# Kernel tuning notes

Hardware: AMD Instinct MI355X
Metric: run time of the kernel (lower is better)

Reference implementation:

```python
import jax, jax.numpy as jnp
import numpy as np

B, T, C = 2, 2048, 1024
N = 16
D = C // N  # 64


def setup_inputs() -> dict:
    key = jax.random.key(0)
    ks = jax.random.split(key, 5)
    s = 1.0 / np.sqrt(C)  # lecun_normal-ish scale for Dense kernels
    return {
        "src": jax.random.normal(ks[0], (B, T, C), jnp.float32),
        "mask": jnp.ones((B, T), jnp.float32),  # unused on causal path
        "Wq": jax.random.normal(ks[1], (C, C), jnp.float32) * s,
        "bq": jnp.zeros((C,), jnp.float32),
        "Wk": jax.random.normal(ks[2], (C, C), jnp.float32) * s,
        "bk": jnp.zeros((C,), jnp.float32),
        "Wv": jax.random.normal(ks[3], (C, C), jnp.float32) * s,
        "bv": jnp.zeros((C,), jnp.float32),
        "Wo": jax.random.normal(ks[4], (C, C), jnp.float32) * s,
        "bo": jnp.zeros((C,), jnp.float32),
    }


def reference(src, mask, Wq, bq, Wk, bk, Wv, bv, Wo, bo):
    # QKV projections -> [B, N, T, D]
    def heads(x):
        return x.reshape(B, T, N, D).transpose(0, 2, 1, 3)

    q = heads(src @ Wq + bq)
    k = heads(src @ Wk + bk)
    v = heads(src @ Wv + bv)

    # scores [B, N, T, T], causal mask, softmax
    scores = jnp.einsum("bntd,bnsd->bnts", q, k) / jnp.sqrt(jnp.float32(D))
    causal = jnp.tril(jnp.ones((T, T), bool))
    scores = jnp.where(causal, scores, -jnp.inf)
    attn = jax.nn.softmax(scores, axis=-1)

    # weighted values, merge heads, output projection (dropout deterministic)
    out = jnp.einsum("bnts,bnsd->bntd", attn, v)
    out = out.transpose(0, 2, 1, 3).reshape(B, T, C)
    return out @ Wo + bo
```

## Files before the change

kernel.cpp:

```cpp
#include <hip/hip_runtime.h>

typedef __bf16 bf16;
typedef bf16 bf16x8 __attribute__((ext_vector_type(8)));
typedef float f32x4 __attribute__((ext_vector_type(4)));
typedef unsigned short u16;
typedef u16 u16x4 __attribute__((ext_vector_type(4)));
typedef u16 u16x8 __attribute__((ext_vector_type(8)));

typedef const __attribute__((address_space(1))) void* gptr_t;
typedef __attribute__((address_space(3))) void* sptr_t;

__device__ __forceinline__ void async16(const void* g, void* l) {
  __builtin_amdgcn_global_load_lds((gptr_t)g, (sptr_t)l, 16, 0, 0);
}
__device__ __forceinline__ u16 f2bf(float v) {
  return __builtin_bit_cast(u16, (bf16)v);
}

__device__ __forceinline__ size_t paddr(int r, int k, int KT) {
  return (size_t)((r >> 4) * KT + (k >> 5)) * 512 + ((k >> 3) & 3) * 128 +
         (r & 15) * 8 + (k & 7);
}

__global__ void kPrep(const float* __restrict__ src, u16* __restrict__ Xp,
                      const float* __restrict__ Wq, const float* __restrict__ Wk,
                      const float* __restrict__ Wv, const float* __restrict__ Wo,
                      u16* __restrict__ Wp) {
  __shared__ float tile[32][33];
  const int bid = blockIdx.x, tid = threadIdx.x;
  if (bid < 4096) {
    const int i = (bid * 256 + tid) * 4;
    const int m = i >> 10, k = i & 1023;
    float4 v = *(const float4*)&src[i];
    u16x4 o = {f2bf(v.x), f2bf(v.y), f2bf(v.z), f2bf(v.w)};
    *(u16x4*)&Xp[paddr(m, k, 32)] = o;
  } else {
    const int t = bid - 4096;
    const int z = t >> 10, tt = t & 1023;
    const float* W = (z == 0) ? Wq : (z == 1) ? Wk : (z == 2) ? Wv : Wo;
    const int n0 = (tt & 31) * 32, k0 = (tt >> 5) * 32;
    const int tx = tid & 31, ty = tid >> 5;
#pragma unroll
    for (int j = 0; j < 4; ++j)
      tile[ty + j * 8][tx] = W[(size_t)(k0 + ty + j * 8) * 1024 + n0 + tx];
    __syncthreads();
    if (tid < 128) {
      const int sub = tid >> 6, l = tid & 63, hi = l >> 4, lo = l & 15;
      u16x8 o;
#pragma unroll
      for (int e = 0; e < 8; ++e) o[e] = f2bf(tile[hi * 8 + e][sub * 16 + lo]);
      const size_t ad = (size_t)z * 1048576 +
                        (size_t)(((n0 >> 4) + sub) * 32 + (k0 >> 5)) * 512 +
                        hi * 128 + lo * 8;
      *(u16x8*)&Wp[ad] = o;
    }
  }
}

__global__ __launch_bounds__(256, 3) void kGemmQKV(
    const u16* __restrict__ A, const u16* __restrict__ Bt,
    const float* __restrict__ b0, const float* __restrict__ b1,
    const float* __restrict__ b2, u16* __restrict__ outQ) {
  __shared__ __align__(16) u16 Als[2][8 * 512];
  const int tid = threadIdx.x, l = tid & 63, w = tid >> 6;
  const int bid = (blockIdx.x & 7) * 96 + (blockIdx.x >> 3);
  const int mb = bid & 31, nb = bid >> 5;
  const int mbase = mb * 128, nbase = nb * 128;
  const int wr = (w >> 1) * 64, wc = (w & 1) * 64;
  const int hi = l >> 4, lo = l & 15;

  const u16* bb[4];
#pragma unroll
  for (int nf = 0; nf < 4; ++nf)
    bb[nf] = &Bt[(size_t)((nbase + wc + nf * 16) >> 4) * 16384 + l * 8];

  f32x4 acc[4][4];
#pragma unroll
  for (int i = 0; i < 4; ++i)
#pragma unroll
    for (int j = 0; j < 4; ++j) acc[i][j] = (f32x4){0.f, 0.f, 0.f, 0.f};

  auto stageA = [&](int bufi, int kt) {
#pragma unroll
    for (int i = 0; i < 2; ++i) {
      const int fr = w * 2 + i;
      async16(&A[(size_t)((mb * 8 + fr) * 32 + kt) * 512 + l * 8],
              &Als[bufi][fr * 512]);
    }
  };

  bf16x8 breg[2][4];
  stageA(0, 0);
#pragma unroll
  for (int nf = 0; nf < 4; ++nf) breg[0][nf] = *(const bf16x8*)&bb[nf][0];

  auto step = [&](int kt, bf16x8 (&bc)[4], bf16x8 (&bn)[4]) {
    const int cur = kt & 1;
    if (kt < 31) {
      stageA(cur ^ 1, kt + 1);
#pragma unroll
      for (int nf = 0; nf < 4; ++nf)
        bn[nf] = *(const bf16x8*)&bb[nf][(kt + 1) * 512];
      asm volatile("s_waitcnt vmcnt(6)" ::: "memory");
    } else {
      asm volatile("s_waitcnt vmcnt(0)" ::: "memory");
    }
    __builtin_amdgcn_s_barrier();
    __builtin_amdgcn_sched_barrier(0);

    bf16x8 a[4];
#pragma unroll
    for (int mf = 0; mf < 4; ++mf)
      a[mf] = *(const bf16x8*)&Als[cur][((w >> 1) * 4 + mf) * 512 + l * 8];
#pragma unroll
    for (int mf = 0; mf < 4; ++mf)
#pragma unroll
      for (int nf = 0; nf < 4; ++nf)
        acc[mf][nf] = __builtin_amdgcn_mfma_f32_16x16x32_bf16(a[mf], bc[nf],
                                                              acc[mf][nf], 0, 0, 0);
    __builtin_amdgcn_s_barrier();
  };

  for (int kt2 = 0; kt2 < 32; kt2 += 2) {
    step(kt2, breg[0], breg[1]);
    step(kt2 + 1, breg[1], breg[0]);
  }

  u16* Qo = outQ;
  u16* Ko = outQ + 4 * 1048576;
  u16* Vo = outQ + 8 * 1048576;
  const int mat = nb >> 3;
  const float* bias = (mat == 0) ? b0 : (mat == 1) ? b1 : b2;
  const float qs = (mat == 0) ? 0.1803368801f : 1.0f;
#pragma unroll
  for (int nf = 0; nf < 4; ++nf) {
    const int n = nbase + wc + nf * 16 + lo;
    const int cc = n & 1023, h = cc >> 6, d = cc & 63;
    const float bsv = bias[cc];
#pragma unroll
    for (int mf = 0; mf < 4; ++mf)
#pragma unroll
      for (int r = 0; r < 4; ++r) {
        const int m = mbase + wr + mf * 16 + hi * 4 + r;
        const int bb_ = m >> 11, t = m & 2047;
        const u16 hv = f2bf((acc[mf][nf][r] + bsv) * qs);
        const size_t hd = (size_t)(bb_ * 16 + h) * 131072;
        if (mat < 2) {
          (mat == 0 ? Qo : Ko)[hd + paddr(t, d, 2)] = hv;
        } else {
          Vo[hd + paddr(d, t, 64)] = hv;
        }
      }
  }
}

__global__ __launch_bounds__(256, 2) void kGemmO(
    const u16* __restrict__ A, const u16* __restrict__ Bt,
    const float* __restrict__ b0, float* __restrict__ outF) {
  __shared__ __align__(16) u16 Als[2][8 * 512];
  const int tid = threadIdx.x, l = tid & 63, w = tid >> 6;
  const int bid = (blockIdx.x & 7) * 64 + (blockIdx.x >> 3);
  const int mb = bid & 31, nb = bid >> 5;
  const int mbase = mb * 128, nbase = nb * 64;
  const int wr = (w >> 1) * 64, wc = (w & 1) * 32;
  const int hi = l >> 4, lo = l & 15;

  const u16* bb[2];
#pragma unroll
  for (int nf = 0; nf < 2; ++nf)
    bb[nf] = &Bt[(size_t)((nbase + wc + nf * 16) >> 4) * 16384 + l * 8];

  f32x4 acc[4][2];
#pragma unroll
  for (int i = 0; i < 4; ++i)
#pragma unroll
    for (int j = 0; j < 2; ++j) acc[i][j] = (f32x4){0.f, 0.f, 0.f, 0.f};

  auto stageA = [&](int bufi, int kt) {
#pragma unroll
    for (int i = 0; i < 2; ++i) {
      const int fr = w * 2 + i;
      async16(&A[(size_t)((mb * 8 + fr) * 32 + kt) * 512 + l * 8],
              &Als[bufi][fr * 512]);
    }
  };

  bf16x8 breg[2][2];
  stageA(0, 0);
#pragma unroll
  for (int nf = 0; nf < 2; ++nf) breg[0][nf] = *(const bf16x8*)&bb[nf][0];

  auto step = [&](int kt, bf16x8 (&bc)[2], bf16x8 (&bn)[2]) {
    const int cur = kt & 1;
    if (kt < 31) {
      stageA(cur ^ 1, kt + 1);
#pragma unroll
      for (int nf = 0; nf < 2; ++nf)
        bn[nf] = *(const bf16x8*)&bb[nf][(kt + 1) * 512];
      asm volatile("s_waitcnt vmcnt(4)" ::: "memory");
    } else {
      asm volatile("s_waitcnt vmcnt(0)" ::: "memory");
    }
    __builtin_amdgcn_s_barrier();
    __builtin_amdgcn_sched_barrier(0);

    bf16x8 a[4];
#pragma unroll
    for (int mf = 0; mf < 4; ++mf)
      a[mf] = *(const bf16x8*)&Als[cur][((w >> 1) * 4 + mf) * 512 + l * 8];
#pragma unroll
    for (int mf = 0; mf < 4; ++mf)
#pragma unroll
      for (int nf = 0; nf < 2; ++nf)
        acc[mf][nf] = __builtin_amdgcn_mfma_f32_16x16x32_bf16(a[mf], bc[nf],
                                                              acc[mf][nf], 0, 0, 0);
    __builtin_amdgcn_s_barrier();
  };

  for (int kt2 = 0; kt2 < 32; kt2 += 2) {
    step(kt2, breg[0], breg[1]);
    step(kt2 + 1, breg[1], breg[0]);
  }

#pragma unroll
  for (int nf = 0; nf < 2; ++nf) {
    const int n = nbase + wc + nf * 16 + lo;
    const float bsv = b0[n];
#pragma unroll
    for (int mf = 0; mf < 4; ++mf)
#pragma unroll
      for (int r = 0; r < 4; ++r) {
        const int m = mbase + wr + mf * 16 + hi * 4 + r;
        outF[(size_t)m * 1024 + n] = acc[mf][nf][r] + bsv;
      }
  }
}

#define PSTR 36
__global__ __launch_bounds__(512, 4) void kAttn(const u16* __restrict__ Qp,
                                                const u16* __restrict__ Kp,
                                                const u16* __restrict__ Vp,
                                                u16* __restrict__ AOp) {
  __shared__ __align__(16) u16 Pl[8][16 * PSTR];
  __shared__ __align__(16) float Red[4][2][16][64];
  __shared__ float RedL[4][2][64];
  const int tid = threadIdx.x, l = tid & 63, w = tid >> 6;
  const int grp = w >> 1, half = w & 1;
  const int g = l >> 4, c = l & 15;
  const int pi = blockIdx.x, bh = blockIdx.y;
  const int qtA = pi, qtB = 31 - pi;
  const size_t head = (size_t)bh * 131072;
  const u16* Kh = Kp + head;
  const u16* Vh = Vp + head;

  bf16x8 aqA[2], aqB[2];
#pragma unroll
  for (int ks = 0; ks < 2; ++ks) {
    aqA[ks] = *(const bf16x8*)&Qp[head + (size_t)((qtA * 4 + grp) * 2 + ks) * 512 + l * 8];
    aqB[ks] = *(const bf16x8*)&Qp[head + (size_t)((qtB * 4 + grp) * 2 + ks) * 512 + l * 8];
  }

  f32x4 accA[4], accB[4];
#pragma unroll
  for (int i = 0; i < 4; ++i) {
    accA[i] = (f32x4){0.f, 0.f, 0.f, 0.f};
    accB[i] = (f32x4){0.f, 0.f, 0.f, 0.f};
  }
  float lA_ = 0.f, lB_ = 0.f;

  bf16x8 kr[4];
#pragma unroll
  for (int f = 0; f < 4; ++f)
    kr[f] = *(const bf16x8*)&Kh[(size_t)((half * 2 + (f >> 1)) * 2 + (f & 1)) * 512 + l * 8];
  bf16x8 vr[4];

  auto finishTile = [&](const f32x4* sT, bool diag, f32x4* accO, float& lpart) {
    float v[8];
#pragma unroll
    for (int sf = 0; sf < 2; ++sf)
#pragma unroll
      for (int r = 0; r < 4; ++r) v[sf * 4 + r] = sT[sf][r];
    if (diag) {
      const int qin = grp * 16 + c;
#pragma unroll
      for (int sf = 0; sf < 2; ++sf)
#pragma unroll
        for (int r = 0; r < 4; ++r)
          if (half * 32 + sf * 16 + g * 4 + r > qin) v[sf * 4 + r] = -__builtin_inff();
    }
    float p[8];
#pragma unroll
    for (int i = 0; i < 8; ++i) p[i] = __builtin_exp2f(v[i]);
#pragma unroll
    for (int sf = 0; sf < 2; ++sf) {
      u16x4 q4 = {f2bf(p[sf * 4 + 0]), f2bf(p[sf * 4 + 1]),
                  f2bf(p[sf * 4 + 2]), f2bf(p[sf * 4 + 3])};
      *(u16x4*)&Pl[w][c * PSTR + sf * 16 + g * 4] = q4;
    }
    lpart += ((p[0] + p[1]) + (p[2] + p[3])) + ((p[4] + p[5]) + (p[6] + p[7]));
    bf16x8 pf = *(const bf16x8*)&Pl[w][c * PSTR + g * 8];
#pragma unroll
    for (int nd = 0; nd < 4; ++nd)
      accO[nd] = __builtin_amdgcn_mfma_f32_16x16x32_bf16(pf, vr[nd], accO[nd], 0, 0, 0);
  };

  for (int st = 0; st <= qtB; ++st) {
#pragma unroll
    for (int nd = 0; nd < 4; ++nd)
      vr[nd] = *(const bf16x8*)&Vh[(size_t)(nd * 64 + st * 2 + half) * 512 + l * 8];
    const bool pair = (st <= qtA);

    f32x4 sB[2], sA[2];
#pragma unroll
    for (int i = 0; i < 2; ++i) {
      sB[i] = (f32x4){0.f, 0.f, 0.f, 0.f};
      sA[i] = (f32x4){0.f, 0.f, 0.f, 0.f};
    }
#pragma unroll
    for (int sf = 0; sf < 2; ++sf)
#pragma unroll
      for (int ks = 0; ks < 2; ++ks)
        sB[sf] = __builtin_amdgcn_mfma_f32_16x16x32_bf16(kr[sf * 2 + ks], aqB[ks],
                                                         sB[sf], 0, 0, 0);
    if (pair)
#pragma unroll
      for (int sf = 0; sf < 2; ++sf)
#pragma unroll
        for (int ks = 0; ks < 2; ++ks)
          sA[sf] = __builtin_amdgcn_mfma_f32_16x16x32_bf16(kr[sf * 2 + ks], aqA[ks],
                                                           sA[sf], 0, 0, 0);
    if (st < qtB) {
#pragma unroll
      for (int f = 0; f < 4; ++f)
        kr[f] = *(const bf16x8*)&Kh[(size_t)(((st + 1) * 4 + half * 2 + (f >> 1)) * 2 +
                                             (f & 1)) * 512 + l * 8];
    }
    finishTile(sB, st == qtB, accB, lB_);
    if (pair) finishTile(sA, st == qtA, accA, lA_);
  }

  float lcB = lB_ + __shfl_xor(lB_, 16);
  lcB += __shfl_xor(lcB, 32);
  float lcA = lA_ + __shfl_xor(lA_, 16);
  lcA += __shfl_xor(lcA, 32);
  __syncthreads();
  if (half) {
#pragma unroll
    for (int nd = 0; nd < 4; ++nd)
#pragma unroll
      for (int r = 0; r < 4; ++r) {
        Red[grp][0][nd * 4 + r][l] = accB[nd][r];
        Red[grp][1][nd * 4 + r][l] = accA[nd][r];
      }
    RedL[grp][0][l] = lcB;
    RedL[grp][1][l] = lcA;
  }
  __syncthreads();
  if (!half) {
#pragma unroll
    for (int nd = 0; nd < 4; ++nd)
#pragma unroll
      for (int r = 0; r < 4; ++r) {
        accB[nd][r] += Red[grp][0][nd * 4 + r][l];
        accA[nd][r] += Red[grp][1][nd * 4 + r][l];
      }
    lcB += RedL[grp][0][l];
    lcA += RedL[grp][1][l];

    const int b = bh >> 4, h = bh & 15;
    auto writeOut = [&](int qt, f32x4* accO, float lc) {
#pragma unroll
      for (int r = 0; r < 4; ++r) {
        const float lr = __shfl(lc, g * 4 + r);
        const float rin = 1.0f / lr;
        const int mg = b * 2048 + qt * 64 + grp * 16 + g * 4 + r;
#pragma unroll
        for (int nd = 0; nd < 4; ++nd) {
          const int col = h * 64 + nd * 16 + c;
          AOp[paddr(mg, col, 32)] = f2bf(accO[nd][r] * rin);
        }
      }
    };
    writeOut(qtB, accB, lcB);
    writeOut(qtA, accA, lcA);
  }
}

extern "C" void kernel_launch(void* const* d_in, const int* in_sizes, int n_in,
                              void* d_out, int out_size, void* d_ws, size_t ws_size,
                              hipStream_t stream) {
  const float* src = (const float*)d_in[0];
  const float* Wq = (const float*)d_in[2];
  const float* bq = (const float*)d_in[3];
  const float* Wk = (const float*)d_in[4];
  const float* bk = (const float*)d_in[5];
  const float* Wv = (const float*)d_in[6];
  const float* bv = (const float*)d_in[7];
  const float* Wo = (const float*)d_in[8];
  const float* bo = (const float*)d_in[9];
  float* out = (float*)d_out;

  char* ws = (char*)d_ws;
  u16* Wp = (u16*)(ws);
  u16* Xp = (u16*)(ws + 8ull * 1024 * 1024);
  u16* Qb = (u16*)(ws + 16ull * 1024 * 1024);
  u16* AOp = (u16*)(ws + 40ull * 1024 * 1024);

  kPrep<<<dim3(8192), dim3(256), 0, stream>>>(src, Xp, Wq, Wk, Wv, Wo, Wp);
  kGemmQKV<<<dim3(768), dim3(256), 0, stream>>>(Xp, Wp, bq, bk, bv, Qb);
  kAttn<<<dim3(16, 32), dim3(512), 0, stream>>>(Qb, Qb + 4 * 1048576,
                                                Qb + 8 * 1048576, AOp);
  kGemmO<<<dim3(512), dim3(256), 0, stream>>>(AOp, Wp + 3ull * 1048576, bo, out);
}
```

Baseline: 116.7 us.

## Process four query tiles per attention block to reuse K/V loads

Each attention block now handles four causally balanced query tiles (pi, 15-pi, 16+pi, 31-pi) instead of two, so every K and V fragment loaded from global memory feeds up to four QK and PV tile computations. The grid shrinks from 512 to 256 blocks and uses a 1D index that maps heads across XCDs so blocks sharing a head stay on the same XCD's L2. Launch bounds drop to 2 blocks per CU to make room for the extra Q fragments and accumulators. The cost is fewer resident waves and a smaller grid, which may reduce latency hiding and leave CUs idle.

```diff
diff --git a/kernel.cpp b/kernel.cpp
--- a/kernel.cpp
+++ b/kernel.cpp
@@ -237,7 +237,7 @@
 }
 
 #define PSTR 36
-__global__ __launch_bounds__(512, 4) void kAttn(const u16* __restrict__ Qp,
+__global__ __launch_bounds__(512, 2) void kAttn(const u16* __restrict__ Qp,
                                                 const u16* __restrict__ Kp,
                                                 const u16* __restrict__ Vp,
                                                 u16* __restrict__ AOp) {
@@ -247,32 +247,47 @@
   const int tid = threadIdx.x, l = tid & 63, w = tid >> 6;
   const int grp = w >> 1, half = w & 1;
   const int g = l >> 4, c = l & 15;
-  const int pi = blockIdx.x, bh = blockIdx.y;
-  const int qtA = pi, qtB = 31 - pi;
+  const int id = blockIdx.x;
+  const int xcd = id & 7, rem = id >> 3;
+  const int pi = rem & 7, bh = (rem >> 3) * 8 + xcd;
+  const int qt0 = 31 - pi, qt1 = 16 + pi, qt2 = 15 - pi, qt3 = pi;
   const size_t head = (size_t)bh * 131072;
   const u16* Kh = Kp + head;
   const u16* Vh = Vp + head;
 
-  bf16x8 aqA[2], aqB[2];
+  bf16x8 aq0[2], aq1[2], aq2[2], aq3[2];
 #pragma unroll
   for (int ks = 0; ks < 2; ++ks) {
-    aqA[ks] = *(const bf16x8*)&Qp[head + (size_t)((qtA * 4 + grp) * 2 + ks) * 512 + l * 8];
-    aqB[ks] = *(const bf16x8*)&Qp[head + (size_t)((qtB * 4 + grp) * 2 + ks) * 512 + l * 8];
-  }
-
-  f32x4 accA[4], accB[4];
+    aq0[ks] = *(const bf16x8*)&Qp[head + (size_t)((qt0 * 4 + grp) * 2 + ks) * 512 + l * 8];
+    aq1[ks] = *(const bf16x8*)&Qp[head + (size_t)((qt1 * 4 + grp) * 2 + ks) * 512 + l * 8];
+    aq2[ks] = *(const bf16x8*)&Qp[head + (size_t)((qt2 * 4 + grp) * 2 + ks) * 512 + l * 8];
+    aq3[ks] = *(const bf16x8*)&Qp[head + (size_t)((qt3 * 4 + grp) * 2 + ks) * 512 + l * 8];
+  }
+
+  f32x4 acc0[4], acc1[4], acc2[4], acc3[4];
 #pragma unroll
   for (int i = 0; i < 4; ++i) {
-    accA[i] = (f32x4){0.f, 0.f, 0.f, 0.f};
-    accB[i] = (f32x4){0.f, 0.f, 0.f, 0.f};
-  }
-  float lA_ = 0.f, lB_ = 0.f;
+    acc0[i] = (f32x4){0.f, 0.f, 0.f, 0.f};
+    acc1[i] = (f32x4){0.f, 0.f, 0.f, 0.f};
+    acc2[i] = (f32x4){0.f, 0.f, 0.f, 0.f};
+    acc3[i] = (f32x4){0.f, 0.f, 0.f, 0.f};
+  }
+  float l0 = 0.f, l1 = 0.f, l2 = 0.f, l3 = 0.f;
 
   bf16x8 kr[4];
 #pragma unroll
   for (int f = 0; f < 4; ++f)
     kr[f] = *(const bf16x8*)&Kh[(size_t)((half * 2 + (f >> 1)) * 2 + (f & 1)) * 512 + l * 8];
   bf16x8 vr[4];
+
+  auto qkTile = [&](const bf16x8* aq, f32x4* sT) {
+#pragma unroll
+    for (int sf = 0; sf < 2; ++sf)
+#pragma unroll
+      for (int ks = 0; ks < 2; ++ks)
+        sT[sf] = __builtin_amdgcn_mfma_f32_16x16x32_bf16(kr[sf * 2 + ks], aq[ks],
+                                                         sT[sf], 0, 0, 0);
+  };
 
   auto finishTile = [&](const f32x4* sT, bool diag, f32x4* accO, float& lpart) {
     float v[8];
@@ -304,86 +319,92 @@
       accO[nd] = __builtin_amdgcn_mfma_f32_16x16x32_bf16(pf, vr[nd], accO[nd], 0, 0, 0);
   };
 
-  for (int st = 0; st <= qtB; ++st) {
+  const int nst = qt0 + 1;
+  for (int st = 0; st < nst; ++st) {
 #pragma unroll
     for (int nd = 0; nd < 4; ++nd)
       vr[nd] = *(const bf16x8*)&Vh[(size_t)(nd * 64 + st * 2 + half) * 512 + l * 8];
-    const bool pair = (st <= qtA);
-
-    f32x4 sB[2], sA[2];
-#pragma unroll
-    for (int i = 0; i < 2; ++i) {
-      sB[i] = (f32x4){0.f, 0.f, 0.f, 0.f};
-      sA[i] = (f32x4){0.f, 0.f, 0.f, 0.f};
-    }
-#pragma unroll
-    for (int sf = 0; sf < 2; ++sf)
-#pragma unroll
-      for (int ks = 0; ks < 2; ++ks)
-        sB[sf] = __builtin_amdgcn_mfma_f32_16x16x32_bf16(kr[sf * 2 + ks], aqB[ks],
-                                                         sB[sf], 0, 0, 0);
-    if (pair)
-#pragma unroll
-      for (int sf = 0; sf < 2; ++sf)
-#pragma unroll
-        for (int ks = 0; ks < 2; ++ks)
-          sA[sf] = __builtin_amdgcn_mfma_f32_16x16x32_bf16(kr[sf * 2 + ks], aqA[ks],
-                                                           sA[sf], 0, 0, 0);
-    if (st < qtB) {
-#pragma unroll
-      for (int f = 0; f < 4; ++f)
-        kr[f] = *(const bf16x8*)&Kh[(size_t)(((st + 1) * 4 + half * 2 + (f >> 1)) * 2 +
-                                             (f & 1)) * 512 + l * 8];
-    }
-    finishTile(sB, st == qtB, accB, lB_);
-    if (pair) finishTile(sA, st == qtA, accA, lA_);
-  }
-
-  float lcB = lB_ + __shfl_xor(lB_, 16);
-  lcB += __shfl_xor(lcB, 32);
-  float lcA = lA_ + __shfl_xor(lA_, 16);
-  lcA += __shfl_xor(lcA, 32);
-  __syncthreads();
-  if (half) {
-#pragma unroll
-    for (int nd = 0; nd < 4; ++nd)
-#pragma unroll
-      for (int r = 0; r < 4; ++r) {
-        Red[grp][0][nd * 4 + r][l] = accB[nd][r];
-        Red[grp][1][nd * 4 + r][l] = accA[nd][r];
+
+    f32x4 sT[2];
+    if (st <= qt3) {
+#pragma unroll
+      for (int i = 0; i < 2; ++i) sT[i] = (f32x4){0.f, 0.f, 0.f, 0.f};
+      qkTile(aq3, sT);
+      finishTile(sT, st == qt3, acc3, l3);
+    }
+    if (st <= qt2) {
+#pragma unroll
+      for (int i = 0; i < 2; ++i) sT[i] = (f32x4){0.f, 0.f, 0.f, 0.f};
+      qkTile(aq2, sT);
+      finishTile(sT, st == qt2, acc2, l2);
+    }
+    if (st <= qt1) {
+#pragma unroll
+      for (int i = 0; i < 2; ++i) sT[i] = (f32x4){0.f, 0.f, 0.f, 0.f};
+      qkTile(aq1, sT);
+      finishTile(sT, st == qt1, acc1, l1);
+    }
+    {
+#pragma unroll
+      for (int i = 0; i < 2; ++i) sT[i] = (f32x4){0.f, 0.f, 0.f, 0.f};
+      qkTile(aq0, sT);
+      if (st < qt0) {
+#pragma unroll
+        for (int f = 0; f < 4; ++f)
+          kr[f] = *(const bf16x8*)&Kh[(size_t)(((st + 1) * 4 + half * 2 + (f >> 1)) * 2 +
+                                               (f & 1)) * 512 + l * 8];
       }
-    RedL[grp][0][l] = lcB;
-    RedL[grp][1][l] = lcA;
-  }
-  __syncthreads();
-  if (!half) {
-#pragma unroll
-    for (int nd = 0; nd < 4; ++nd)
-#pragma unroll
-      for (int r = 0; r < 4; ++r) {
-        accB[nd][r] += Red[grp][0][nd * 4 + r][l];
-        accA[nd][r] += Red[grp][1][nd * 4 + r][l];
+      finishTile(sT, st == qt0, acc0, l0);
+    }
+  }
+
+  const int b = bh >> 4, h = bh & 15;
+  auto writeOut = [&](int qt, const f32x4* accO, float lc) {
+#pragma unroll
+    for (int r = 0; r < 4; ++r) {
+      const float lr = __shfl(lc, g * 4 + r);
+      const float rin = 1.0f / lr;
+      const int mg = b * 2048 + qt * 64 + grp * 16 + g * 4 + r;
+#pragma unroll
+      for (int nd = 0; nd < 4; ++nd) {
+        const int col = h * 64 + nd * 16 + c;
+        AOp[paddr(mg, col, 32)] = f2bf(accO[nd][r] * rin);
       }
-    lcB += RedL[grp][0][l];
-    lcA += RedL[grp][1][l];
-
-    const int b = bh >> 4, h = bh & 15;
-    auto writeOut = [&](int qt, f32x4* accO, float lc) {
-#pragma unroll
-      for (int r = 0; r < 4; ++r) {
-        const float lr = __shfl(lc, g * 4 + r);
-        const float rin = 1.0f / lr;
-        const int mg = b * 2048 + qt * 64 + grp * 16 + g * 4 + r;
-#pragma unroll
-        for (int nd = 0; nd < 4; ++nd) {
-          const int col = h * 64 + nd * 16 + c;
-          AOp[paddr(mg, col, 32)] = f2bf(accO[nd][r] * rin);
+    }
+  };
+  auto combinePair = [&](f32x4* accX, float lX, int qtX, f32x4* accY, float lY,
+                         int qtY) {
+    float lcX = lX + __shfl_xor(lX, 16);
+    lcX += __shfl_xor(lcX, 32);
+    float lcY = lY + __shfl_xor(lY, 16);
+    lcY += __shfl_xor(lcY, 32);
+    __syncthreads();
+    if (half) {
+#pragma unroll
+      for (int nd = 0; nd < 4; ++nd)
+#pragma unroll
+        for (int r = 0; r < 4; ++r) {
+          Red[grp][0][nd * 4 + r][l] = accX[nd][r];
+          Red[grp][1][nd * 4 + r][l] = accY[nd][r];
         }
-      }
-    };
-    writeOut(qtB, accB, lcB);
-    writeOut(qtA, accA, lcA);
-  }
+      RedL[grp][0][l] = lcX;
+      RedL[grp][1][l] = lcY;
+    }
+    __syncthreads();
+    if (!half) {
+#pragma unroll
+      for (int nd = 0; nd < 4; ++nd)
+#pragma unroll
+        for (int r = 0; r < 4; ++r) {
+          accX[nd][r] += Red[grp][0][nd * 4 + r][l];
+          accY[nd][r] += Red[grp][1][nd * 4 + r][l];
+        }
+      writeOut(qtX, accX, lcX + RedL[grp][0][l]);
+      writeOut(qtY, accY, lcY + RedL[grp][1][l]);
+    }
+  };
+  combinePair(acc0, l0, qt0, acc1, l1, qt1);
+  combinePair(acc2, l2, qt2, acc3, l3, qt3);
 }
 
 extern "C" void kernel_launch(void* const* d_in, const int* in_sizes, int n_in,
@@ -408,7 +429,7 @@
 
   kPrep<<<dim3(8192), dim3(256), 0, stream>>>(src, Xp, Wq, Wk, Wv, Wo, Wp);
   kGemmQKV<<<dim3(768), dim3(256), 0, stream>>>(Xp, Wp, bq, bk, bv, Qb);
-  kAttn<<<dim3(16, 32), dim3(512), 0, stream>>>(Qb, Qb + 4 * 1048576,
-                                                Qb + 8 * 1048576, AOp);
+  kAttn<<<dim3(256), dim3(512), 0, stream>>>(Qb, Qb + 4 * 1048576,
+                                             Qb + 8 * 1048576, AOp);
   kGemmO<<<dim3(512), dim3(256), 0, stream>>>(AOp, Wp + 3ull * 1048576, bo, out);
 }
```

Result: faster. 104.3 us (-10.7%).
